# Optimization experiments

Hardware: AMD Instinct MI355X
Metric: run time of the kernel (lower is better)

The kernel has to match this reference:

```python
import jax, jax.numpy as jnp
import numpy as np

N_NODES = 100000


def _gcn_norm(edge_index, num_nodes):
    # add self loops
    src, dst = edge_index[0], edge_index[1]
    loop = jnp.arange(num_nodes, dtype=src.dtype)
    row = jnp.concatenate([src, loop])  # [E+N]
    col = jnp.concatenate([dst, loop])
    ew = jnp.ones(row.shape[0], dtype=jnp.float32)
    deg = jax.ops.segment_sum(ew, col, num_segments=num_nodes)  # [N]
    dinv = jnp.where(deg > 0, jax.lax.rsqrt(deg), 0.0)
    norm = dinv[row] * ew * dinv[col]  # [E+N]
    return row, col, norm


def setup_inputs() -> dict:
    key = jax.random.key(0)
    k1, k2, k3 = jax.random.split(key, 3)
    x = jax.random.normal(k1, (N_NODES, 64), dtype=jnp.float32)
    edge_index = jax.random.randint(k2, (2, 1280000), 0, N_NODES, dtype=jnp.int64)
    W = jax.random.normal(k3, (40, 64), dtype=jnp.float32) * (1.0 / np.sqrt(64))
    b = jnp.zeros((40,), dtype=jnp.float32)
    return {"x": x, "edge_index": edge_index, "W": W, "b": b}


def reference(x, edge_index, W, b):
    K = 3
    row, col, norm = _gcn_norm(edge_index, N_NODES)
    h = x
    for _ in range(K):
        # gather from source nodes, scale by symmetric norm, scatter-add to dst
        msg = norm[:, None] * h[row]  # [E+N, F]
        h = jax.ops.segment_sum(msg, col, num_segments=N_NODES)
    logits = h @ W.T + b  # [N, C]
    return jax.nn.log_softmax(logits, axis=1)
```

## Files before the change

### kernel.cpp

```cpp
#include <hip/hip_runtime.h>

#define F_IN 64
#define F_OUT 40
#define QPN 5
#define LOQ4 4

#define PART_BLK 256
#define PART_EPB 8
#define PART_TILE (PART_BLK * PART_EPB)
#define BSHIFT 8
#define BCAP 4096
#define MAXB 512

#define WSTRIDE 17
#define NPB 51

__device__ inline unsigned pk2(float x, float y) {
    unsigned a = __float_as_uint(x); a = (a + 0x7FFFu + ((a >> 16) & 1u)) >> 16;
    unsigned b = __float_as_uint(y); b = (b + 0x7FFFu + ((b >> 16) & 1u)) >> 16;
    return a | (b << 16);
}
__device__ inline void up2(unsigned u, float& a, float& b) {
    a = __uint_as_float(u << 16); b = __uint_as_float(u & 0xFFFF0000u);
}

#define ACC8(V) do { float b0_, b1_; \
    up2((V).x, b0_, b1_); a0 += b0_; a1 += b1_; \
    up2((V).y, b0_, b1_); a2 += b0_; a3 += b1_; \
    up2((V).z, b0_, b1_); a4 += b0_; a5 += b1_; \
    up2((V).w, b0_, b1_); a6 += b0_; a7 += b1_; } while (0)

__global__ __launch_bounds__(PART_BLK) void partition_kernel(const int* __restrict__ src,
                                                             const int* __restrict__ dst,
                                                             int* __restrict__ bfill,
                                                             unsigned* __restrict__ staging,
                                                             int E, int nbk) {
    __shared__ int hist[MAXB];
    __shared__ int base[MAXB];
    int tid = threadIdx.x;
    for (int b = tid; b < nbk; b += PART_BLK) hist[b] = 0;
    __syncthreads();

    int rank[PART_EPB];
    int bk[PART_EPB];
    unsigned rec[PART_EPB];
    int eb = blockIdx.x * PART_TILE + tid;
#pragma unroll
    for (int k = 0; k < PART_EPB; ++k) {
        int e = eb + k * PART_BLK;
        if (e < E) {
            int r = src[e];
            int c = dst[e];
            int b = c >> BSHIFT;
            bk[k] = b;
            rec[k] = (unsigned)r | ((unsigned)(c & 255) << 17);
            rank[k] = atomicAdd(&hist[b], 1);
        } else {
            bk[k] = -1;
        }
    }
    __syncthreads();
    for (int b = tid; b < nbk; b += PART_BLK) {
        int h = hist[b];
        base[b] = h ? (b * BCAP + atomicAdd(&bfill[b], h)) : 0;
    }
    __syncthreads();
#pragma unroll
    for (int k = 0; k < PART_EPB; ++k) {
        if (bk[k] >= 0) staging[base[bk[k]] + rank[k]] = rec[k];
    }
}

__global__ __launch_bounds__(512) void bucket_finalize_kernel(const unsigned* __restrict__ staging,
                                                              const int* __restrict__ bfill,
                                                              int* __restrict__ rowptr,
                                                              float* __restrict__ dinv,
                                                              float* __restrict__ dinv2,
                                                              int* __restrict__ srcs, int n, int E) {
    int b = blockIdx.x;
    __shared__ int h[256];
    __shared__ int cur[256];
    __shared__ int sbase;
    int tid = threadIdx.x;
    if (tid < 256) h[tid] = 0;
    if (tid == 0) sbase = 0;
    __syncthreads();

    int part = 0;
    for (int j = tid; j < b; j += 512) part += bfill[j];
    if (part) atomicAdd(&sbase, part);

    int cnt = bfill[b];
    const unsigned* rec = staging + (size_t)b * BCAP;
    for (int i = tid; i < cnt; i += 512) {
        atomicAdd(&h[rec[i] >> 17], 1);
    }
    __syncthreads();

    int base = sbase;
    int v = (tid < 256) ? h[tid] : 0;
    for (int off = 1; off < 256; off <<= 1) {
        int t = (tid >= off && tid < 256) ? h[tid - off] : 0;
        __syncthreads();
        if (tid < 256) h[tid] += t;
        __syncthreads();
    }
    if (tid < 256) {
        int excl = h[tid] - v;
        int node = (b << BSHIFT) | tid;
        if (node < n) {
            rowptr[node] = base + excl;
            float r = rsqrtf((float)v + 1.0f);
            dinv[node] = r;
            dinv2[node] = r * r;
        }
        cur[tid] = base + excl;
    }
    if (b == 0 && tid == 0) rowptr[n] = E;
    __syncthreads();

    for (int i = tid; i < cnt; i += 512) {
        unsigned rv = rec[i];
        int pos = atomicAdd(&cur[rv >> 17], 1);
        srcs[pos] = (int)(rv & 0x1FFFFu);
    }
}

__global__ __launch_bounds__(256, 4) void proj_kernel(const float* __restrict__ x,
                                                      const float* __restrict__ W,
                                                      const float* __restrict__ dinv,
                                                      unsigned* __restrict__ ulo,
                                                      unsigned* __restrict__ uhi, int n) {
    __shared__ float Ws[F_OUT * WSTRIDE * 4];
    for (int i = threadIdx.x; i < F_OUT * F_IN; i += 256) {
        int c = i >> 6;
        int k = i & 63;
        Ws[c * (WSTRIDE * 4) + k] = W[i];
    }
    __syncthreads();

    int t = blockIdx.x * 256 + threadIdx.x;
    int g = t >> 2;
    int q = t & 3;
    int n0 = 2 * g;
    if (n0 >= n) return;
    int n1 = n0 + 1;

    const float4* xp0 = (const float4*)(x + (size_t)n0 * F_IN);
    const float4* xp1 = (const float4*)(x + (size_t)n1 * F_IN);
    const float4* Wq  = (const float4*)Ws + (size_t)(q * 10) * WSTRIDE;

    float acc0[10], acc1[10];
#pragma unroll
    for (int c = 0; c < 10; ++c) { acc0[c] = 0.0f; acc1[c] = 0.0f; }

#pragma unroll 1
    for (int f4 = 0; f4 < F_IN / 4; ++f4) {
        float4 x0 = xp0[f4];
        float4 x1 = xp1[f4];
#pragma unroll
        for (int c = 0; c < 10; ++c) {
            float4 w = Wq[c * WSTRIDE + f4];
            acc0[c] += x0.x * w.x + x0.y * w.y + x0.z * w.z + x0.w * w.w;
            acc1[c] += x1.x * w.x + x1.y * w.y + x1.z * w.z + x1.w * w.w;
        }
    }

    float d0 = dinv[n0];
    float d1 = dinv[n1];
#pragma unroll
    for (int j = 0; j < 5; ++j) {
        int idx = q * 5 + j;
        unsigned w0 = pk2(d0 * acc0[2 * j], d0 * acc0[2 * j + 1]);
        unsigned w1 = pk2(d1 * acc1[2 * j], d1 * acc1[2 * j + 1]);
        if (idx < 16) {
            ulo[(size_t)n0 * 16 + idx] = w0;
            ulo[(size_t)n1 * 16 + idx] = w1;
        } else {
            uhi[(size_t)n0 * 4 + (idx - 16)] = w0;
            uhi[(size_t)n1 * 4 + (idx - 16)] = w1;
        }
    }
}

__global__ __launch_bounds__(256) void propagate_kernel(const int* __restrict__ rowptr,
                                                        const int* __restrict__ srcs,
                                                        const float* __restrict__ dinv2,
                                                        const unsigned* __restrict__ ulo_c,
                                                        const unsigned* __restrict__ uhi_c,
                                                        unsigned* __restrict__ ulo_n,
                                                        unsigned* __restrict__ uhi_n, int n) {
    int t = blockIdx.x * blockDim.x + threadIdx.x;
    int node = t / QPN;
    int q = t - node * QPN;
    if (node >= n) return;

    int beg = rowptr[node];
    int end = rowptr[node + 1];

    bool hi = (q == 4);
    const uint4* U = hi ? (const uint4*)uhi_c : (const uint4*)ulo_c;
    int sh = hi ? 0 : 2;
    int off = hi ? 0 : q;

    uint4 sv = U[((size_t)node << sh) + off];
    float a0, a1, a2, a3, a4, a5, a6, a7;
    up2(sv.x, a0, a1); up2(sv.y, a2, a3); up2(sv.z, a4, a5); up2(sv.w, a6, a7);

    int i = beg;
    for (; i + 3 < end; i += 4) {
        int s0 = srcs[i], s1 = srcs[i + 1], s2 = srcs[i + 2], s3 = srcs[i + 3];
        uint4 v0 = U[((size_t)s0 << sh) + off];
        uint4 v1 = U[((size_t)s1 << sh) + off];
        uint4 v2 = U[((size_t)s2 << sh) + off];
        uint4 v3 = U[((size_t)s3 << sh) + off];
        ACC8(v0); ACC8(v1); ACC8(v2); ACC8(v3);
    }
    for (; i < end; ++i) {
        uint4 v = U[((size_t)srcs[i] << sh) + off];
        ACC8(v);
    }

    float ds = dinv2[node];
    uint4 o;
    o.x = pk2(ds * a0, ds * a1);
    o.y = pk2(ds * a2, ds * a3);
    o.z = pk2(ds * a4, ds * a5);
    o.w = pk2(ds * a6, ds * a7);
    uint4* Un = hi ? (uint4*)uhi_n : (uint4*)ulo_n;
    Un[((size_t)node << sh) + off] = o;
}

__global__ __launch_bounds__(256) void propagate_lsm_kernel(const int* __restrict__ rowptr,
                                                            const int* __restrict__ srcs,
                                                            const float* __restrict__ dinv,
                                                            const unsigned* __restrict__ ulo_c,
                                                            const unsigned* __restrict__ uhi_c,
                                                            const float* __restrict__ bias,
                                                            float* __restrict__ out, int n) {
    __shared__ float red[256];
    int tid = threadIdx.x;
    int gl = tid / QPN;
    int q  = tid - gl * QPN;
    int node = blockIdx.x * NPB + gl;
    bool active = (gl < NPB) && (node < n);

    float a0 = 0, a1 = 0, a2 = 0, a3 = 0, a4 = 0, a5 = 0, a6 = 0, a7 = 0;
    float dv = 0.0f;
    if (active) {
        int beg = rowptr[node];
        int end = rowptr[node + 1];
        bool hi = (q == 4);
        const uint4* U = hi ? (const uint4*)uhi_c : (const uint4*)ulo_c;
        int sh = hi ? 0 : 2;
        int off = hi ? 0 : q;
        uint4 sv = U[((size_t)node << sh) + off];
        up2(sv.x, a0, a1); up2(sv.y, a2, a3); up2(sv.z, a4, a5); up2(sv.w, a6, a7);
        int i = beg;
        for (; i + 3 < end; i += 4) {
            int s0 = srcs[i], s1 = srcs[i + 1], s2 = srcs[i + 2], s3 = srcs[i + 3];
            uint4 v0 = U[((size_t)s0 << sh) + off];
            uint4 v1 = U[((size_t)s1 << sh) + off];
            uint4 v2 = U[((size_t)s2 << sh) + off];
            uint4 v3 = U[((size_t)s3 << sh) + off];
            ACC8(v0); ACC8(v1); ACC8(v2); ACC8(v3);
        }
        for (; i < end; ++i) {
            uint4 v = U[((size_t)srcs[i] << sh) + off];
            ACC8(v);
        }
        dv = dinv[node];
    }

    float y0 = dv * a0 + bias[q * 8 + 0];
    float y1 = dv * a1 + bias[q * 8 + 1];
    float y2 = dv * a2 + bias[q * 8 + 2];
    float y3 = dv * a3 + bias[q * 8 + 3];
    float y4 = dv * a4 + bias[q * 8 + 4];
    float y5 = dv * a5 + bias[q * 8 + 5];
    float y6 = dv * a6 + bias[q * 8 + 6];
    float y7 = dv * a7 + bias[q * 8 + 7];

    float pm = fmaxf(fmaxf(fmaxf(y0, y1), fmaxf(y2, y3)),
                     fmaxf(fmaxf(y4, y5), fmaxf(y6, y7)));
    red[tid] = active ? pm : -1e30f;
    __syncthreads();
    int base = tid - q;
    float mx = fmaxf(fmaxf(fmaxf(red[base], red[base + 1]), fmaxf(red[base + 2], red[base + 3])),
                     red[base + 4]);
    __syncthreads();
    float ps = __expf(y0 - mx) + __expf(y1 - mx) + __expf(y2 - mx) + __expf(y3 - mx)
             + __expf(y4 - mx) + __expf(y5 - mx) + __expf(y6 - mx) + __expf(y7 - mx);
    red[tid] = active ? ps : 0.0f;
    __syncthreads();
    float se = red[base] + red[base + 1] + red[base + 2] + red[base + 3] + red[base + 4];
    float lse = mx + __logf(se);

    if (active) {
        float4* p = (float4*)(out + (size_t)node * F_OUT + q * 8);
        float4 o0, o1;
        o0.x = y0 - lse; o0.y = y1 - lse; o0.z = y2 - lse; o0.w = y3 - lse;
        o1.x = y4 - lse; o1.y = y5 - lse; o1.z = y6 - lse; o1.w = y7 - lse;
        p[0] = o0;
        p[1] = o1;
    }
}

extern "C" void kernel_launch(void* const* d_in, const int* in_sizes, int n_in,
                              void* d_out, int out_size, void* d_ws, size_t ws_size,
                              hipStream_t stream) {
    const float* x  = (const float*)d_in[0];
    const int*   ei = (const int*)d_in[1];
    const float* W  = (const float*)d_in[2];
    const float* b  = (const float*)d_in[3];

    const int N = in_sizes[0] / F_IN;
    const int E = in_sizes[1] / 2;
    const int* src = ei;
    const int* dst = ei + E;
    const int nbk = (N + (1 << BSHIFT) - 1) >> BSHIFT;

    char* base = (char*)d_ws;
    size_t off = 0;
    auto alloc = [&](size_t bytes) {
        char* p = base + off;
        off = (off + bytes + 255) & ~(size_t)255;
        return p;
    };
    float*    dinv    = (float*)   alloc((size_t)N * 4);
    float*    dinv2   = (float*)   alloc((size_t)N * 4);
    int*      rowptr  = (int*)     alloc((size_t)(N + 1) * 4);
    int*      bfill   = (int*)     alloc((size_t)MAXB * 4);
    unsigned* staging = (unsigned*)alloc((size_t)nbk * BCAP * 4);
    int*      srcs_s  = (int*)     alloc((size_t)E * 4);
    unsigned* uloA    = (unsigned*)alloc((size_t)N * 16 * 4);
    unsigned* uhiA    = (unsigned*)alloc((size_t)N * 4 * 4);
    unsigned* uloB    = (unsigned*)alloc((size_t)N * 16 * 4);
    unsigned* uhiB    = (unsigned*)alloc((size_t)N * 4 * 4);
    float*    outp    = (float*)d_out;

    hipMemsetAsync(bfill, 0, (size_t)MAXB * 4, stream);
    partition_kernel<<<(E + PART_TILE - 1) / PART_TILE, PART_BLK, 0, stream>>>(
        src, dst, bfill, staging, E, nbk);

    bucket_finalize_kernel<<<nbk, 512, 0, stream>>>(staging, bfill, rowptr,
                                                    dinv, dinv2, srcs_s, N, E);

    proj_kernel<<<((size_t)N * 2 + 255) / 256, 256, 0, stream>>>(x, W, dinv, uloA, uhiA, N);

    const int pt = N * QPN;
    const int pg = (pt + 255) / 256;
    propagate_kernel<<<pg, 256, 0, stream>>>(rowptr, srcs_s, dinv2, uloA, uhiA, uloB, uhiB, N);
    propagate_kernel<<<pg, 256, 0, stream>>>(rowptr, srcs_s, dinv2, uloB, uhiB, uloA, uhiA, N);

    const int fb = (N + NPB - 1) / NPB;
    propagate_lsm_kernel<<<fb, 256, 0, stream>>>(rowptr, srcs_s, dinv, uloA, uhiA, b, outp, N);
}
```

Before: 221.0 us.

## Split propagation into two 20-column halves to shrink gather working set

The 40-column bf16 feature table is split into two 20-column tables, each with 40-byte rows. All three hops run on one half and then on the other, with each thread gathering a uint2 instead of a uint4. The aim is for each half's working set (about 4MB) to fit better in cache during the random gathers. The cost is that the CSR index arrays are traversed twice as many times. The final hop now writes pre-softmax logits to the output, and a separate log-softmax kernel reads them back, adding launches and an extra pass over the output.

```diff
diff --git a/kernel.cpp b/kernel.cpp
--- a/kernel.cpp
+++ b/kernel.cpp
@@ -3,7 +3,7 @@
 #define F_IN 64
 #define F_OUT 40
 #define QPN 5
-#define LOQ4 4
+#define UROW 10
 
 #define PART_BLK 256
 #define PART_EPB 8
@@ -24,11 +24,9 @@
     a = __uint_as_float(u << 16); b = __uint_as_float(u & 0xFFFF0000u);
 }
 
-#define ACC8(V) do { float b0_, b1_; \
+#define ACC4(V) do { float b0_, b1_; \
     up2((V).x, b0_, b1_); a0 += b0_; a1 += b1_; \
-    up2((V).y, b0_, b1_); a2 += b0_; a3 += b1_; \
-    up2((V).z, b0_, b1_); a4 += b0_; a5 += b1_; \
-    up2((V).w, b0_, b1_); a6 += b0_; a7 += b1_; } while (0)
+    up2((V).y, b0_, b1_); a2 += b0_; a3 += b1_; } while (0)
 
 __global__ __launch_bounds__(PART_BLK) void partition_kernel(const int* __restrict__ src,
                                                              const int* __restrict__ dst,
@@ -129,8 +127,8 @@
 __global__ __launch_bounds__(256, 4) void proj_kernel(const float* __restrict__ x,
                                                       const float* __restrict__ W,
                                                       const float* __restrict__ dinv,
-                                                      unsigned* __restrict__ ulo,
-                                                      unsigned* __restrict__ uhi, int n) {
+                                                      unsigned* __restrict__ u0,
+                                                      unsigned* __restrict__ u1, int n) {
     __shared__ float Ws[F_OUT * WSTRIDE * 4];
     for (int i = threadIdx.x; i < F_OUT * F_IN; i += 256) {
         int c = i >> 6;
@@ -168,28 +166,22 @@
 
     float d0 = dinv[n0];
     float d1 = dinv[n1];
+    unsigned* buf = (q >> 1) ? u1 : u0;
+    int base = (q & 1) * 5;
+    unsigned* up0 = buf + (size_t)n0 * UROW + base;
+    unsigned* up1 = buf + (size_t)n1 * UROW + base;
 #pragma unroll
     for (int j = 0; j < 5; ++j) {
-        int idx = q * 5 + j;
-        unsigned w0 = pk2(d0 * acc0[2 * j], d0 * acc0[2 * j + 1]);
-        unsigned w1 = pk2(d1 * acc1[2 * j], d1 * acc1[2 * j + 1]);
-        if (idx < 16) {
-            ulo[(size_t)n0 * 16 + idx] = w0;
-            ulo[(size_t)n1 * 16 + idx] = w1;
-        } else {
-            uhi[(size_t)n0 * 4 + (idx - 16)] = w0;
-            uhi[(size_t)n1 * 4 + (idx - 16)] = w1;
-        }
+        up0[j] = pk2(d0 * acc0[2 * j], d0 * acc0[2 * j + 1]);
+        up1[j] = pk2(d1 * acc1[2 * j], d1 * acc1[2 * j + 1]);
     }
 }
 
 __global__ __launch_bounds__(256) void propagate_kernel(const int* __restrict__ rowptr,
                                                         const int* __restrict__ srcs,
                                                         const float* __restrict__ dinv2,
-                                                        const unsigned* __restrict__ ulo_c,
-                                                        const unsigned* __restrict__ uhi_c,
-                                                        unsigned* __restrict__ ulo_n,
-                                                        unsigned* __restrict__ uhi_n, int n) {
+                                                        const unsigned* __restrict__ ucur,
+                                                        unsigned* __restrict__ unew, int n) {
     int t = blockIdx.x * blockDim.x + threadIdx.x;
     int node = t / QPN;
     int q = t - node * QPN;
@@ -198,46 +190,77 @@
     int beg = rowptr[node];
     int end = rowptr[node + 1];
 
-    bool hi = (q == 4);
-    const uint4* U = hi ? (const uint4*)uhi_c : (const uint4*)ulo_c;
-    int sh = hi ? 0 : 2;
-    int off = hi ? 0 : q;
-
-    uint4 sv = U[((size_t)node << sh) + off];
-    float a0, a1, a2, a3, a4, a5, a6, a7;
-    up2(sv.x, a0, a1); up2(sv.y, a2, a3); up2(sv.z, a4, a5); up2(sv.w, a6, a7);
+    const uint2* U = (const uint2*)ucur;
+    uint2 sv = U[(size_t)node * QPN + q];
+    float a0, a1, a2, a3;
+    up2(sv.x, a0, a1); up2(sv.y, a2, a3);
 
     int i = beg;
     for (; i + 3 < end; i += 4) {
         int s0 = srcs[i], s1 = srcs[i + 1], s2 = srcs[i + 2], s3 = srcs[i + 3];
-        uint4 v0 = U[((size_t)s0 << sh) + off];
-        uint4 v1 = U[((size_t)s1 << sh) + off];
-        uint4 v2 = U[((size_t)s2 << sh) + off];
-        uint4 v3 = U[((size_t)s3 << sh) + off];
-        ACC8(v0); ACC8(v1); ACC8(v2); ACC8(v3);
+        uint2 v0 = U[(size_t)s0 * QPN + q];
+        uint2 v1 = U[(size_t)s1 * QPN + q];
+        uint2 v2 = U[(size_t)s2 * QPN + q];
+        uint2 v3 = U[(size_t)s3 * QPN + q];
+        ACC4(v0); ACC4(v1); ACC4(v2); ACC4(v3);
     }
     for (; i < end; ++i) {
-        uint4 v = U[((size_t)srcs[i] << sh) + off];
-        ACC8(v);
+        uint2 v = U[(size_t)srcs[i] * QPN + q];
+        ACC4(v);
     }
 
     float ds = dinv2[node];
-    uint4 o;
+    uint2 o;
     o.x = pk2(ds * a0, ds * a1);
     o.y = pk2(ds * a2, ds * a3);
-    o.z = pk2(ds * a4, ds * a5);
-    o.w = pk2(ds * a6, ds * a7);
-    uint4* Un = hi ? (uint4*)uhi_n : (uint4*)ulo_n;
-    Un[((size_t)node << sh) + off] = o;
-}
-
-__global__ __launch_bounds__(256) void propagate_lsm_kernel(const int* __restrict__ rowptr,
-                                                            const int* __restrict__ srcs,
-                                                            const float* __restrict__ dinv,
-                                                            const unsigned* __restrict__ ulo_c,
-                                                            const unsigned* __restrict__ uhi_c,
-                                                            const float* __restrict__ bias,
-                                                            float* __restrict__ out, int n) {
+    ((uint2*)unew)[(size_t)node * QPN + q] = o;
+}
+
+__global__ __launch_bounds__(256) void hop3_kernel(const int* __restrict__ rowptr,
+                                                   const int* __restrict__ srcs,
+                                                   const float* __restrict__ dinv,
+                                                   const unsigned* __restrict__ ucur,
+                                                   const float* __restrict__ bias,
+                                                   float* __restrict__ out, int n, int pbase) {
+    int t = blockIdx.x * blockDim.x + threadIdx.x;
+    int node = t / QPN;
+    int q = t - node * QPN;
+    if (node >= n) return;
+
+    int beg = rowptr[node];
+    int end = rowptr[node + 1];
+
+    const uint2* U = (const uint2*)ucur;
+    uint2 sv = U[(size_t)node * QPN + q];
+    float a0, a1, a2, a3;
+    up2(sv.x, a0, a1); up2(sv.y, a2, a3);
+
+    int i = beg;
+    for (; i + 3 < end; i += 4) {
+        int s0 = srcs[i], s1 = srcs[i + 1], s2 = srcs[i + 2], s3 = srcs[i + 3];
+        uint2 v0 = U[(size_t)s0 * QPN + q];
+        uint2 v1 = U[(size_t)s1 * QPN + q];
+        uint2 v2 = U[(size_t)s2 * QPN + q];
+        uint2 v3 = U[(size_t)s3 * QPN + q];
+        ACC4(v0); ACC4(v1); ACC4(v2); ACC4(v3);
+    }
+    for (; i < end; ++i) {
+        uint2 v = U[(size_t)srcs[i] * QPN + q];
+        ACC4(v);
+    }
+
+    float dv = dinv[node];
+    int cb = pbase + q * 4;
+    float4 y;
+    y.x = dv * a0 + bias[cb + 0];
+    y.y = dv * a1 + bias[cb + 1];
+    y.z = dv * a2 + bias[cb + 2];
+    y.w = dv * a3 + bias[cb + 3];
+    *(float4*)(out + (size_t)node * F_OUT + cb) = y;
+}
+
+__global__ __launch_bounds__(256) void lsm_kernel(float* __restrict__ out,
+                                                  int n) {
     __shared__ float red[256];
     int tid = threadIdx.x;
     int gl = tid / QPN;
@@ -245,41 +268,14 @@
     int node = blockIdx.x * NPB + gl;
     bool active = (gl < NPB) && (node < n);
 
-    float a0 = 0, a1 = 0, a2 = 0, a3 = 0, a4 = 0, a5 = 0, a6 = 0, a7 = 0;
-    float dv = 0.0f;
+    float y0 = 0, y1 = 0, y2 = 0, y3 = 0, y4 = 0, y5 = 0, y6 = 0, y7 = 0;
+    float4* p = (float4*)(out + (size_t)node * F_OUT + q * 8);
     if (active) {
-        int beg = rowptr[node];
-        int end = rowptr[node + 1];
-        bool hi = (q == 4);
-        const uint4* U = hi ? (const uint4*)uhi_c : (const uint4*)ulo_c;
-        int sh = hi ? 0 : 2;
-        int off = hi ? 0 : q;
-        uint4 sv = U[((size_t)node << sh) + off];
-        up2(sv.x, a0, a1); up2(sv.y, a2, a3); up2(sv.z, a4, a5); up2(sv.w, a6, a7);
-        int i = beg;
-        for (; i + 3 < end; i += 4) {
-            int s0 = srcs[i], s1 = srcs[i + 1], s2 = srcs[i + 2], s3 = srcs[i + 3];
-            uint4 v0 = U[((size_t)s0 << sh) + off];
-            uint4 v1 = U[((size_t)s1 << sh) + off];
-            uint4 v2 = U[((size_t)s2 << sh) + off];
-            uint4 v3 = U[((size_t)s3 << sh) + off];
-            ACC8(v0); ACC8(v1); ACC8(v2); ACC8(v3);
-        }
-        for (; i < end; ++i) {
-            uint4 v = U[((size_t)srcs[i] << sh) + off];
-            ACC8(v);
-        }
-        dv = dinv[node];
-    }
-
-    float y0 = dv * a0 + bias[q * 8 + 0];
-    float y1 = dv * a1 + bias[q * 8 + 1];
-    float y2 = dv * a2 + bias[q * 8 + 2];
-    float y3 = dv * a3 + bias[q * 8 + 3];
-    float y4 = dv * a4 + bias[q * 8 + 4];
-    float y5 = dv * a5 + bias[q * 8 + 5];
-    float y6 = dv * a6 + bias[q * 8 + 6];
-    float y7 = dv * a7 + bias[q * 8 + 7];
+        float4 r0 = p[0];
+        float4 r1 = p[1];
+        y0 = r0.x; y1 = r0.y; y2 = r0.z; y3 = r0.w;
+        y4 = r1.x; y5 = r1.y; y6 = r1.z; y7 = r1.w;
+    }
 
     float pm = fmaxf(fmaxf(fmaxf(y0, y1), fmaxf(y2, y3)),
                      fmaxf(fmaxf(y4, y5), fmaxf(y6, y7)));
@@ -297,7 +293,6 @@
     float lse = mx + __logf(se);
 
     if (active) {
-        float4* p = (float4*)(out + (size_t)node * F_OUT + q * 8);
         float4 o0, o1;
         o0.x = y0 - lse; o0.y = y1 - lse; o0.z = y2 - lse; o0.w = y3 - lse;
         o1.x = y4 - lse; o1.y = y5 - lse; o1.z = y6 - lse; o1.w = y7 - lse;
@@ -333,10 +328,10 @@
     int*      bfill   = (int*)     alloc((size_t)MAXB * 4);
     unsigned* staging = (unsigned*)alloc((size_t)nbk * BCAP * 4);
     int*      srcs_s  = (int*)     alloc((size_t)E * 4);
-    unsigned* uloA    = (unsigned*)alloc((size_t)N * 16 * 4);
-    unsigned* uhiA    = (unsigned*)alloc((size_t)N * 4 * 4);
-    unsigned* uloB    = (unsigned*)alloc((size_t)N * 16 * 4);
-    unsigned* uhiB    = (unsigned*)alloc((size_t)N * 4 * 4);
+    unsigned* uA0     = (unsigned*)alloc((size_t)N * UROW * 4);
+    unsigned* uB0     = (unsigned*)alloc((size_t)N * UROW * 4);
+    unsigned* uA1     = (unsigned*)alloc((size_t)N * UROW * 4);
+    unsigned* uB1     = (unsigned*)alloc((size_t)N * UROW * 4);
     float*    outp    = (float*)d_out;
 
     hipMemsetAsync(bfill, 0, (size_t)MAXB * 4, stream);
@@ -346,13 +341,19 @@
     bucket_finalize_kernel<<<nbk, 512, 0, stream>>>(staging, bfill, rowptr,
                                                     dinv, dinv2, srcs_s, N, E);
 
-    proj_kernel<<<((size_t)N * 2 + 255) / 256, 256, 0, stream>>>(x, W, dinv, uloA, uhiA, N);
+    proj_kernel<<<((size_t)N * 2 + 255) / 256, 256, 0, stream>>>(x, W, dinv, uA0, uA1, N);
 
     const int pt = N * QPN;
     const int pg = (pt + 255) / 256;
-    propagate_kernel<<<pg, 256, 0, stream>>>(rowptr, srcs_s, dinv2, uloA, uhiA, uloB, uhiB, N);
-    propagate_kernel<<<pg, 256, 0, stream>>>(rowptr, srcs_s, dinv2, uloB, uhiB, uloA, uhiA, N);
-
     const int fb = (N + NPB - 1) / NPB;
-    propagate_lsm_kernel<<<fb, 256, 0, stream>>>(rowptr, srcs_s, dinv, uloA, uhiA, b, outp, N);
-}
+
+    propagate_kernel<<<pg, 256, 0, stream>>>(rowptr, srcs_s, dinv2, uA0, uB0, N);
+    propagate_kernel<<<pg, 256, 0, stream>>>(rowptr, srcs_s, dinv2, uB0, uA0, N);
+    hop3_kernel<<<pg, 256, 0, stream>>>(rowptr, srcs_s, dinv, uA0, b, outp, N, 0);
+
+    propagate_kernel<<<pg, 256, 0, stream>>>(rowptr, srcs_s, dinv2, uA1, uB1, N);
+    propagate_kernel<<<pg, 256, 0, stream>>>(rowptr, srcs_s, dinv2, uB1, uA1, N);
+    hop3_kernel<<<pg, 256, 0, stream>>>(rowptr, srcs_s, dinv, uA1, b, outp, N, 20);
+
+    lsm_kernel<<<fb, 256, 0, stream>>>(outp, N);
+}
```

Measured after the change: 246.8 us. 1.12x slower.
